# Optimization experiments

Measured on AMD Instinct MI355X. Metric: run time of the kernel, lower is better.

Reference implementation:

```python
import jax, jax.numpy as jnp
import numpy as np

D_MODEL = 2048
N_HEADS = 16
KV_HEADS = 4
HEAD_DIM = D_MODEL // N_HEADS  # 128
GROUPS = N_HEADS // KV_HEADS   # 4
CLIP_QKV = 8.0
EPS = 1e-5
MAX_POS = 2048
ROPE_THETA = 10000.0


def _make_rope(max_pos, dim, theta):
    inv_freq = 1.0 / (theta ** (np.arange(0, dim, 2, dtype=np.float32) / dim))
    t = np.arange(max_pos, dtype=np.float32)
    freqs = np.outer(t, inv_freq)                      # [max_pos, dim/2]
    emb = np.concatenate([freqs, freqs], axis=-1)      # [max_pos, dim]
    return jnp.asarray(np.sin(emb)), jnp.asarray(np.cos(emb))


def setup_inputs() -> dict:
    key = jax.random.key(0)
    ks = jax.random.split(key, 6)
    B, S = 2, 2048
    hidden_states = jax.random.normal(ks[0], (B, S, D_MODEL), dtype=jnp.float32)
    attention_mask = jnp.ones((B, S), dtype=jnp.int32)
    position_ids = jnp.broadcast_to(jnp.arange(S, dtype=jnp.int32)[None, :], (B, S))
    init_std = 0.02
    qkv_out = D_MODEL + 2 * KV_HEADS * HEAD_DIM
    wqkv = jax.random.normal(ks[1], (D_MODEL, qkv_out), dtype=jnp.float32) * init_std
    w_out = jax.random.normal(ks[2], (D_MODEL, D_MODEL), dtype=jnp.float32) * init_std
    norm1_w = jnp.ones((D_MODEL,), dtype=jnp.float32)
    norm2_w = jnp.ones((D_MODEL,), dtype=jnp.float32)
    rope_sin, rope_cos = _make_rope(MAX_POS, HEAD_DIM, ROPE_THETA)
    return {
        'hidden_states': hidden_states,
        'attention_mask': attention_mask,
        'position_ids': position_ids,
        'wqkv': wqkv,
        'w_out': w_out,
        'norm1_w': norm1_w,
        'norm2_w': norm2_w,
        'rope_sin': rope_sin,
        'rope_cos': rope_cos,
    }


def _rmsnorm(x, w, eps=EPS):
    var = jnp.mean(jnp.square(x), axis=-1, keepdims=True)
    return (x * jax.lax.rsqrt(var + eps)) * w


def _rotate_half(x):
    h = x.shape[-1] // 2
    return jnp.concatenate([-x[..., h:], x[..., :h]], axis=-1)


def reference(hidden_states, attention_mask, position_ids, wqkv, w_out, norm1_w, norm2_w, rope_sin, rope_cos):
    B, S, _ = hidden_states.shape
    residual = hidden_states
    # pre-norm
    x = _rmsnorm(hidden_states, norm1_w)
    # fused QKV projection + clip
    qkv = jnp.clip(x @ wqkv, -CLIP_QKV, CLIP_QKV)
    q = qkv[..., :D_MODEL].reshape(B, S, N_HEADS, HEAD_DIM)
    kv_sz = KV_HEADS * HEAD_DIM
    k = qkv[..., D_MODEL:D_MODEL + kv_sz].reshape(B, S, KV_HEADS, HEAD_DIM)
    v = qkv[..., D_MODEL + kv_sz:].reshape(B, S, KV_HEADS, HEAD_DIM)
    # rotary embedding (bshd layout)
    sin = rope_sin[position_ids][:, :, None, :]  # [B,S,1,hd]
    cos = rope_cos[position_ids][:, :, None, :]
    q = q * cos + _rotate_half(q) * sin
    k = k * cos + _rotate_half(k) * sin
    # GQA head repeat
    k = jnp.repeat(k, GROUPS, axis=2)  # [B,S,H,hd]
    v = jnp.repeat(v, GROUPS, axis=2)
    # attention
    scale = 1.0 / jnp.sqrt(jnp.float32(HEAD_DIM))
    scores = jnp.einsum('bqhd,bkhd->bhqk', q, k) * scale
    causal = jnp.tril(jnp.ones((S, S), dtype=bool))
    mask = causal[None, None, :, :] & (attention_mask[:, None, None, :] > 0)
    scores = jnp.where(mask, scores, jnp.finfo(scores.dtype).min)
    probs = jax.nn.softmax(scores, axis=-1)
    attn = jnp.einsum('bhqk,bkhd->bqhd', probs, v).reshape(B, S, D_MODEL)
    attn = attn @ w_out
    # residual add (resid dropout deterministic -> identity) + post-norm
    hidden = residual + attn
    residual_out = hidden
    post = _rmsnorm(hidden, norm2_w)
    return residual_out, post
```

## Files before the change

kernel.cpp:

```cpp
#include <hip/hip_runtime.h>
#include <cstdint>
#include <cstddef>

#define D_MODEL 2048
#define SEQ     2048
#define NB      2
#define ROWS    4096
#define QKV_N   3072
#define NH      16
#define NKV     4
#define HD      128
#define EPSV    1e-5f
#define QPRE    (0.08838834764831845f * 1.4426950408889634f)

typedef unsigned short ushort_t;
typedef __attribute__((ext_vector_type(8))) short  short8;
typedef __attribute__((ext_vector_type(4))) short  short4v;
typedef __attribute__((ext_vector_type(4))) float  floatx4;

__device__ __forceinline__ ushort_t f2b(float f) {
    unsigned u = __float_as_uint(f);
    u += 0x7fffu + ((u >> 16) & 1u);
    return (ushort_t)(u >> 16);
}
__device__ __forceinline__ float b2f(ushort_t u) {
    return __uint_as_float(((unsigned)u) << 16);
}

__device__ __forceinline__ unsigned pkbf(float lo, float hi) {
    unsigned u0 = __float_as_uint(lo) + 0x8000u;
    unsigned u1 = __float_as_uint(hi) + 0x8000u;
    return __builtin_amdgcn_perm(u1, u0, 0x07060302u);
}

#if __has_builtin(__builtin_amdgcn_mfma_f32_16x16x16bf16_1k)
#define HAVE_1K 1
#endif

__device__ __forceinline__ floatx4 pv_mfma(short4v a, short4v b, floatx4 c) {
#ifdef HAVE_1K
    return __builtin_amdgcn_mfma_f32_16x16x16bf16_1k(a, b, c, 0, 0, 0);
#else
    short8 a8 = {a[0], a[1], a[2], a[3], 0, 0, 0, 0};
    short8 b8 = {b[0], b[1], b[2], b[3], 0, 0, 0, 0};
    return __builtin_amdgcn_mfma_f32_16x16x32_bf16(a8, b8, c, 0, 0, 0);
#endif
}

#define GLD_LDS16(gp, lp) __builtin_amdgcn_global_load_lds( \
    (const __attribute__((address_space(1))) void*)(gp),   \
    (__attribute__((address_space(3))) void*)(lp), 16, 0, 0)

__global__ __launch_bounds__(256) void k_rmsnorm_bf16(
        const float* __restrict__ x, const float* __restrict__ w,
        ushort_t* __restrict__ out) {
    int row = blockIdx.x, t = threadIdx.x;
    const float4* xr = (const float4*)(x + (size_t)row * D_MODEL);
    float4 a = xr[t], b = xr[t + 256];
    float ss = a.x*a.x + a.y*a.y + a.z*a.z + a.w*a.w
             + b.x*b.x + b.y*b.y + b.z*b.z + b.w*b.w;
    for (int m = 1; m < 64; m <<= 1) ss += __shfl_xor(ss, m);
    __shared__ float sred[4];
    if ((t & 63) == 0) sred[t >> 6] = ss;
    __syncthreads();
    float r = rsqrtf((sred[0] + sred[1] + sred[2] + sred[3]) * (1.0f / D_MODEL) + EPSV);
    const float4* wr = (const float4*)w;
    float4 wa = wr[t], wb = wr[t + 256];
    ushort4 pa, pb;
    pa.x = f2b(a.x * r * wa.x); pa.y = f2b(a.y * r * wa.y);
    pa.z = f2b(a.z * r * wa.z); pa.w = f2b(a.w * r * wa.w);
    pb.x = f2b(b.x * r * wb.x); pb.y = f2b(b.y * r * wb.y);
    pb.z = f2b(b.z * r * wb.z); pb.w = f2b(b.w * r * wb.w);
    ushort4* o = (ushort4*)(out + (size_t)row * D_MODEL);
    o[t] = pa; o[t + 256] = pb;
}

__global__ __launch_bounds__(256) void k_rmsnorm_f32(
        const float* __restrict__ x, const float* __restrict__ w,
        float* __restrict__ out) {
    int row = blockIdx.x, t = threadIdx.x;
    const float4* xr = (const float4*)(x + (size_t)row * D_MODEL);
    float4 a = xr[t], b = xr[t + 256];
    float ss = a.x*a.x + a.y*a.y + a.z*a.z + a.w*a.w
             + b.x*b.x + b.y*b.y + b.z*b.z + b.w*b.w;
    for (int m = 1; m < 64; m <<= 1) ss += __shfl_xor(ss, m);
    __shared__ float sred[4];
    if ((t & 63) == 0) sred[t >> 6] = ss;
    __syncthreads();
    float r = rsqrtf((sred[0] + sred[1] + sred[2] + sred[3]) * (1.0f / D_MODEL) + EPSV);
    const float4* wr = (const float4*)w;
    float4 wa = wr[t], wb = wr[t + 256];
    float4 oa, ob;
    oa.x = a.x * r * wa.x; oa.y = a.y * r * wa.y; oa.z = a.z * r * wa.z; oa.w = a.w * r * wa.w;
    ob.x = b.x * r * wb.x; ob.y = b.y * r * wb.y; ob.z = b.z * r * wb.z; ob.w = b.w * r * wb.w;
    float4* o = (float4*)(out + (size_t)row * D_MODEL);
    o[t] = oa; o[t + 256] = ob;
}

__global__ __launch_bounds__(256) void k_transpose_cvt(
        const float* __restrict__ in, ushort_t* __restrict__ out, int R, int C) {
    __shared__ float tile[32][33];
    int bc = blockIdx.x * 32, br = blockIdx.y * 32;
    int t = threadIdx.x, lr = t >> 5, lc = t & 31;
    for (int i = 0; i < 4; i++)
        tile[lr + i * 8][lc] = in[(size_t)(br + lr + i * 8) * C + bc + lc];
    __syncthreads();
    for (int i = 0; i < 4; i++)
        out[(size_t)(bc + lr + i * 8) * R + br + lc] = f2b(tile[lc][lr + i * 8]);
}

template <int MODE>
__global__ __launch_bounds__(256) void k_gemm(
        const ushort_t* __restrict__ A, const ushort_t* __restrict__ Bt,
        void* __restrict__ Cout, const float* __restrict__ resid,
        int M, int N, int K) {
    __shared__ __align__(16) ushort_t sA[128 * 32];
    __shared__ __align__(16) ushort_t sB[128 * 32];
    int bm = blockIdx.y * 128, bn = blockIdx.x * 128;
    int t = threadIdx.x;
    int wv = t >> 6, lane = t & 63;
    int wm = (wv >> 1) * 64, wn = (wv & 1) * 64;
    int q4 = lane >> 4, n16 = lane & 15;

    int srow = lane >> 2, scol = (lane & 3) * 8;
    const ushort_t* gA0 = A  + (size_t)(bm + wv * 32 + srow) * K + scol;
    const ushort_t* gA1 = gA0 + (size_t)16 * K;
    const ushort_t* gB0 = Bt + (size_t)(bn + wv * 32 + srow) * K + scol;
    const ushort_t* gB1 = gB0 + (size_t)16 * K;
    ushort_t* lA0 = sA + wv * 1024;
    ushort_t* lA1 = lA0 + 512;
    ushort_t* lB0 = sB + wv * 1024;
    ushort_t* lB1 = lB0 + 512;

    floatx4 zero4 = {0.0f, 0.0f, 0.0f, 0.0f};
    floatx4 acc[4][4];
    for (int i = 0; i < 4; i++)
        for (int j = 0; j < 4; j++) acc[i][j] = zero4;

    for (int k0 = 0; k0 < K; k0 += 32) {
        GLD_LDS16(gA0 + k0, lA0);
        GLD_LDS16(gA1 + k0, lA1);
        GLD_LDS16(gB0 + k0, lB0);
        GLD_LDS16(gB1 + k0, lB1);
        __syncthreads();
        short8 af[4], bfr[4];
        for (int i = 0; i < 4; i++) af[i]  = *(const short8*)&sA[(wm + i * 16 + n16) * 32 + q4 * 8];
        for (int j = 0; j < 4; j++) bfr[j] = *(const short8*)&sB[(wn + j * 16 + n16) * 32 + q4 * 8];
        for (int i = 0; i < 4; i++)
            for (int j = 0; j < 4; j++)
                acc[i][j] = __builtin_amdgcn_mfma_f32_16x16x32_bf16(af[i], bfr[j], acc[i][j], 0, 0, 0);
        __syncthreads();
    }

    for (int i = 0; i < 4; i++) {
        int rbase = bm + wm + i * 16 + q4 * 4;
        for (int j = 0; j < 4; j++) {
            int col = bn + wn + j * 16 + n16;
            if (MODE == 0) {
                ushort_t* C = (ushort_t*)Cout;
                for (int r = 0; r < 4; r++) {
                    float v = acc[i][j][r];
                    v = fminf(fmaxf(v, -8.0f), 8.0f);
                    C[(size_t)(rbase + r) * N + col] = f2b(v);
                }
            } else {
                float* C = (float*)Cout;
                for (int r = 0; r < 4; r++) {
                    float v = acc[i][j][r] + resid[(size_t)(rbase + r) * N + col];
                    C[(size_t)(rbase + r) * N + col] = v;
                }
            }
        }
    }
}

__global__ __launch_bounds__(256) void k_rope(
        const ushort_t* __restrict__ qkv, const int* __restrict__ pos_ids,
        const float* __restrict__ rsin, const float* __restrict__ rcos,
        ushort_t* __restrict__ qout, ushort_t* __restrict__ kout) {
    int wid  = blockIdx.x * 4 + (threadIdx.x >> 6);
    int lane = threadIdx.x & 63;
    int row = wid / 20, slot = wid - row * 20;
    int b = row >> 11, s = row & 2047;
    int pos = pos_ids[row];
    int col0 = (slot < 16) ? slot * HD : D_MODEL + (slot - 16) * HD;
    const ushort_t* src = qkv + (size_t)row * QKV_N + col0;
    float xl = b2f(src[lane]);
    float xh = b2f(src[lane + 64]);
    const float* cp = rcos + (size_t)pos * HD;
    const float* sp = rsin + (size_t)pos * HD;
    float cl = cp[lane], sl = sp[lane];
    float ch = cp[lane + 64], sh = sp[lane + 64];
    float mul = (slot < 16) ? QPRE : 1.0f;
    float ol = (xl * cl - xh * sl) * mul;
    float oh = (xh * ch + xl * sh) * mul;
    if (slot < 16) {
        size_t dst = ((size_t)(b * NH + slot) * SEQ + s) * HD;
        qout[dst + lane] = f2b(ol); qout[dst + lane + 64] = f2b(oh);
    } else {
        size_t dst = ((size_t)(b * NKV + (slot - 16)) * SEQ + s) * HD;
        kout[dst + lane] = f2b(ol); kout[dst + lane + 64] = f2b(oh);
    }
}

__global__ __launch_bounds__(256) void k_vtrans(
        const ushort_t* __restrict__ qkv, ushort_t* __restrict__ vt) {
    __shared__ ushort_t tile[32][33];
    int bh = blockIdx.z;
    int b = bh >> 2, h = bh & 3;
    int s0 = blockIdx.x * 32, d0 = blockIdx.y * 32;
    int t = threadIdx.x, lr = t >> 5, lc = t & 31;
    int col0 = D_MODEL + NKV * HD + h * HD;
    for (int i = 0; i < 4; i++)
        tile[lr + i * 8][lc] =
            qkv[((size_t)b * SEQ + s0 + lr + i * 8) * QKV_N + col0 + d0 + lc];
    __syncthreads();
    for (int i = 0; i < 4; i++)
        vt[((size_t)bh * HD + d0 + lr + i * 8) * SEQ + s0 + lc] = tile[lc][lr + i * 8];
}

__global__ __launch_bounds__(256, 2) void k_attn(
        const ushort_t* __restrict__ Q, const ushort_t* __restrict__ Kr,
        const ushort_t* __restrict__ Vt, const int* __restrict__ amask,
        ushort_t* __restrict__ O) {
    int bidx = blockIdx.x;
    int qt = (SEQ / 64 - 1) - (bidx >> 5);
    int bh = bidx & 31, h = bh & 15, b = bh >> 4;
    int wave = threadIdx.x >> 6, lane = threadIdx.x & 63;
    int q4 = lane >> 4, n16 = lane & 15;

    __shared__ __align__(16) ushort_t sK[2][64 * 128];
    __shared__ __align__(16) ushort_t sV[2][128 * 64];

    const ushort_t* Qh = Q  + (size_t)bh * SEQ * HD;
    const ushort_t* Kh = Kr + (size_t)(b * NKV + (h >> 2)) * SEQ * HD;
    const ushort_t* Vh = Vt + (size_t)(b * NKV + (h >> 2)) * HD * SEQ;
    const int* am = amask + b * SEQ;

    int q0 = qt * 64 + wave * 16;
    int qcol = q0 + n16;

    short8 qf[4];
    for (int kk = 0; kk < 4; kk++)
        qf[kk] = *(const short8*)(Qh + (size_t)qcol * HD + kk * 32 + q4 * 8);

    floatx4 zero4 = {0.0f, 0.0f, 0.0f, 0.0f};
    floatx4 o_acc[8];
    for (int dt = 0; dt < 8; dt++) o_acc[dt] = zero4;
    float m_i = -INFINITY, l_i = 0.0f;

    int krow_l = (lane >> 4);
    int kc_l   = lane & 15;
    int vrow_l = (lane >> 3);
    int vc_l   = lane & 7;

    auto stage_kv = [&](int buf, int kv0) {
        #pragma unroll
        for (int t = 0; t < 4; t++) {
            int krow = wave * 16 + t * 4 + krow_l;
            int kc   = kc_l ^ (krow & 7);
            GLD_LDS16(Kh + (size_t)(kv0 + krow) * HD + kc * 8,
                      &sK[buf][(wave * 16 + t * 4) * 128]);
            int vrow = wave * 32 + t * 8 + vrow_l;
            int vc   = vc_l ^ (vrow & 7);
            GLD_LDS16(Vh + (size_t)vrow * SEQ + kv0 + vc * 8,
                      &sV[buf][(wave * 32 + t * 8) * 64]);
        }
    };

    int kv_iters = qt + 1;

    stage_kv(0, 0);
    asm volatile("s_waitcnt vmcnt(0)" ::: "memory");
    __builtin_amdgcn_s_barrier();
    __builtin_amdgcn_sched_barrier(0);

    for (int it = 0; it < kv_iters; it++) {
        int cur = it & 1;
        int kv0 = it * 64;
        if (it + 1 < kv_iters)
            stage_kv(cur ^ 1, kv0 + 64);

        const ushort_t* sKc = sK[cur];
        const ushort_t* sVc = sV[cur];

        bool tail = (kv0 + 63 > q0);
        floatx4 st[4];
        for (int jj = 0; jj < 4; jj++) st[jj] = zero4;
        for (int jj = 0; jj < 4; jj++) {
            int krow = jj * 16 + n16;
            int sw = krow & 7;
            const ushort_t* kb = sKc + krow * 128;
            for (int kk = 0; kk < 4; kk++) {
                short8 kf = *(const short8*)(kb + ((kk * 4 + q4) ^ sw) * 8);
                st[jj] = __builtin_amdgcn_mfma_f32_16x16x32_bf16(kf, qf[kk], st[jj], 0, 0, 0);
            }
        }
        for (int jj = 0; jj < 4; jj++) {
            int kvb = kv0 + jj * 16 + q4 * 4;
            int4 am4 = *(const int4*)(am + kvb);
            int amr[4] = {am4.x, am4.y, am4.z, am4.w};
            if (tail) {
                for (int r = 0; r < 4; r++)
                    st[jj][r] = (amr[r] > 0 && kvb + r <= qcol) ? st[jj][r] : -1e30f;
            } else {
                for (int r = 0; r < 4; r++)
                    st[jj][r] = (amr[r] > 0) ? st[jj][r] : -1e30f;
            }
        }
        float mx = st[0][0];
        for (int jj = 0; jj < 4; jj++)
            for (int r = 0; r < 4; r++) mx = fmaxf(mx, st[jj][r]);
        mx = fmaxf(mx, __shfl_xor(mx, 16));
        mx = fmaxf(mx, __shfl_xor(mx, 32));
        if (!__all(mx - m_i <= 8.0f)) {
            float mnew = fmaxf(m_i, mx);
            float al = exp2f(m_i - mnew);
            m_i = mnew;
            l_i *= al;
            for (int dt = 0; dt < 8; dt++)
                o_acc[dt] *= al;
        }
        float rs = 0.0f;
        for (int jj = 0; jj < 4; jj++)
            for (int r = 0; r < 4; r++) {
                float p = exp2f(st[jj][r] - m_i);
                st[jj][r] = p;
                rs += p;
            }
        rs += __shfl_xor(rs, 16);
        rs += __shfl_xor(rs, 32);
        l_i += rs;
        for (int jj = 0; jj < 4; jj++) {
            union { unsigned u[2]; short4v s; } uu;
            uu.u[0] = pkbf(st[jj][0], st[jj][1]);
            uu.u[1] = pkbf(st[jj][2], st[jj][3]);
            short4v pfr = uu.s;
            int ch = jj * 2 + (q4 >> 1), hh = q4 & 1;
            for (int dt = 0; dt < 8; dt++) {
                int vrow = dt * 16 + n16;
                short4v vf = *(const short4v*)(sVc + vrow * 64 + ((ch ^ (vrow & 7)) * 8) + hh * 4);
                o_acc[dt] = pv_mfma(vf, pfr, o_acc[dt]);
            }
        }
        asm volatile("s_waitcnt vmcnt(0)" ::: "memory");
        __builtin_amdgcn_s_barrier();
        __builtin_amdgcn_sched_barrier(0);
    }
    float inv = 1.0f / l_i;
    ushort_t* orow = O + ((size_t)(b * SEQ) + qcol) * D_MODEL + h * HD + q4 * 4;
    for (int dt = 0; dt < 8; dt++) {
        uint2 pk;
        pk.x = pkbf(o_acc[dt][0] * inv, o_acc[dt][1] * inv);
        pk.y = pkbf(o_acc[dt][2] * inv, o_acc[dt][3] * inv);
        *(uint2*)(orow + dt * 16) = pk;
    }
}

extern "C" void kernel_launch(void* const* d_in, const int* in_sizes, int n_in,
                              void* d_out, int out_size, void* d_ws, size_t ws_size,
                              hipStream_t stream) {
    const float* hidden = (const float*)d_in[0];
    const int*   amask  = (const int*)d_in[1];
    const int*   pos    = (const int*)d_in[2];
    const float* wqkv   = (const float*)d_in[3];
    const float* wout   = (const float*)d_in[4];
    const float* n1w    = (const float*)d_in[5];
    const float* n2w    = (const float*)d_in[6];
    const float* rsin   = (const float*)d_in[7];
    const float* rcos   = (const float*)d_in[8];
    float* out0 = (float*)d_out;
    float* out1 = out0 + (size_t)ROWS * D_MODEL;

    char* ws = (char*)d_ws;
    ushort_t* x_bf    = (ushort_t*)ws;  ws += (size_t)ROWS * D_MODEL * 2;
    ushort_t* wqkv_t  = (ushort_t*)ws;  ws += (size_t)QKV_N * D_MODEL * 2;
    ushort_t* wout_t  = (ushort_t*)ws;  ws += (size_t)D_MODEL * D_MODEL * 2;
    ushort_t* qkv     = (ushort_t*)ws;  ws += (size_t)ROWS * QKV_N * 2;
    ushort_t* qrot    = (ushort_t*)ws;  ws += (size_t)NB * NH * SEQ * HD * 2;
    ushort_t* krot    = (ushort_t*)ws;  ws += (size_t)NB * NKV * SEQ * HD * 2;
    ushort_t* vt      = (ushort_t*)ws;  ws += (size_t)NB * NKV * HD * SEQ * 2;
    ushort_t* attn    = (ushort_t*)ws;  ws += (size_t)ROWS * D_MODEL * 2;

    k_rmsnorm_bf16<<<ROWS, 256, 0, stream>>>(hidden, n1w, x_bf);
    k_transpose_cvt<<<dim3(QKV_N / 32, D_MODEL / 32), 256, 0, stream>>>(wqkv, wqkv_t, D_MODEL, QKV_N);
    k_transpose_cvt<<<dim3(D_MODEL / 32, D_MODEL / 32), 256, 0, stream>>>(wout, wout_t, D_MODEL, D_MODEL);
    k_gemm<0><<<dim3(QKV_N / 128, ROWS / 128), 256, 0, stream>>>(x_bf, wqkv_t, qkv, nullptr, ROWS, QKV_N, D_MODEL);
    k_rope<<<ROWS * 20 / 4, 256, 0, stream>>>(qkv, pos, rsin, rcos, qrot, krot);
    k_vtrans<<<dim3(SEQ / 32, HD / 32, NB * NKV), 256, 0, stream>>>(qkv, vt);
    k_attn<<<(SEQ / 64) * 32, 256, 0, stream>>>(qrot, krot, vt, amask, attn);
    k_gemm<1><<<dim3(D_MODEL / 128, ROWS / 128), 256, 0, stream>>>(attn, wout_t, out0, hidden, ROWS, D_MODEL, D_MODEL);
    k_rmsnorm_f32<<<ROWS, 256, 0, stream>>>(out0, n2w, out1);
}
```

Measured before the change: 392.4 us.

## Pair short and long causal query tiles per attention block to balance work

Each attention block now processes two query tiles, p and 31-p, so every block does the same total causal work, and the grid halves to 512 blocks. Each K/V tile staged in LDS is reused for both query tiles while both are active. The aim is to remove the load imbalance and tail effect of the triangular causal workload and to cut K/V staging traffic. In exchange, each thread holds doubled accumulators and Q fragments, which raises register pressure and may lower occupancy under the existing launch bounds of 2.

```diff
diff --git a/kernel.cpp b/kernel.cpp
--- a/kernel.cpp
+++ b/kernel.cpp
@@ -224,7 +224,7 @@
         const ushort_t* __restrict__ Vt, const int* __restrict__ amask,
         ushort_t* __restrict__ O) {
     int bidx = blockIdx.x;
-    int qt = (SEQ / 64 - 1) - (bidx >> 5);
+    int p = bidx >> 5;
     int bh = bidx & 31, h = bh & 15, b = bh >> 4;
     int wave = threadIdx.x >> 6, lane = threadIdx.x & 63;
     int q4 = lane >> 4, n16 = lane & 15;
@@ -237,17 +237,21 @@
     const ushort_t* Vh = Vt + (size_t)(b * NKV + (h >> 2)) * HD * SEQ;
     const int* am = amask + b * SEQ;
 
-    int q0 = qt * 64 + wave * 16;
-    int qcol = q0 + n16;
-
-    short8 qf[4];
-    for (int kk = 0; kk < 4; kk++)
-        qf[kk] = *(const short8*)(Qh + (size_t)qcol * HD + kk * 32 + q4 * 8);
+    int qA0 = p * 64 + wave * 16;
+    int qB0 = (31 - p) * 64 + wave * 16;
+    int qcolA = qA0 + n16, qcolB = qB0 + n16;
+
+    short8 qfA[4], qfB[4];
+    for (int kk = 0; kk < 4; kk++) {
+        qfA[kk] = *(const short8*)(Qh + (size_t)qcolA * HD + kk * 32 + q4 * 8);
+        qfB[kk] = *(const short8*)(Qh + (size_t)qcolB * HD + kk * 32 + q4 * 8);
+    }
 
     floatx4 zero4 = {0.0f, 0.0f, 0.0f, 0.0f};
-    floatx4 o_acc[8];
-    for (int dt = 0; dt < 8; dt++) o_acc[dt] = zero4;
-    float m_i = -INFINITY, l_i = 0.0f;
+    floatx4 oA[8], oB[8];
+    for (int dt = 0; dt < 8; dt++) { oA[dt] = zero4; oB[dt] = zero4; }
+    float mA = -INFINITY, lA = 0.0f;
+    float mB = -INFINITY, lB = 0.0f;
 
     int krow_l = (lane >> 4);
     int kc_l   = lane & 15;
@@ -268,7 +272,7 @@
         }
     };
 
-    int kv_iters = qt + 1;
+    int kv_iters = 32 - p;
 
     stage_kv(0, 0);
     asm volatile("s_waitcnt vmcnt(0)" ::: "memory");
@@ -284,76 +288,157 @@
         const ushort_t* sKc = sK[cur];
         const ushort_t* sVc = sV[cur];
 
-        bool tail = (kv0 + 63 > q0);
-        floatx4 st[4];
-        for (int jj = 0; jj < 4; jj++) st[jj] = zero4;
-        for (int jj = 0; jj < 4; jj++) {
-            int krow = jj * 16 + n16;
-            int sw = krow & 7;
-            const ushort_t* kb = sKc + krow * 128;
-            for (int kk = 0; kk < 4; kk++) {
-                short8 kf = *(const short8*)(kb + ((kk * 4 + q4) ^ sw) * 8);
-                st[jj] = __builtin_amdgcn_mfma_f32_16x16x32_bf16(kf, qf[kk], st[jj], 0, 0, 0);
+        bool activeA = (kv0 <= qA0 + 15);
+        bool tailA = (kv0 + 63 > qA0);
+        bool tailB = (kv0 + 63 > qB0);
+
+        floatx4 stA[4], stB[4];
+        for (int jj = 0; jj < 4; jj++) { stA[jj] = zero4; stB[jj] = zero4; }
+
+        if (activeA) {
+            for (int jj = 0; jj < 4; jj++) {
+                int krow = jj * 16 + n16;
+                int sw = krow & 7;
+                const ushort_t* kb = sKc + krow * 128;
+                for (int kk = 0; kk < 4; kk++) {
+                    short8 kf = *(const short8*)(kb + ((kk * 4 + q4) ^ sw) * 8);
+                    stB[jj] = __builtin_amdgcn_mfma_f32_16x16x32_bf16(kf, qfB[kk], stB[jj], 0, 0, 0);
+                    stA[jj] = __builtin_amdgcn_mfma_f32_16x16x32_bf16(kf, qfA[kk], stA[jj], 0, 0, 0);
+                }
+            }
+        } else {
+            for (int jj = 0; jj < 4; jj++) {
+                int krow = jj * 16 + n16;
+                int sw = krow & 7;
+                const ushort_t* kb = sKc + krow * 128;
+                for (int kk = 0; kk < 4; kk++) {
+                    short8 kf = *(const short8*)(kb + ((kk * 4 + q4) ^ sw) * 8);
+                    stB[jj] = __builtin_amdgcn_mfma_f32_16x16x32_bf16(kf, qfB[kk], stB[jj], 0, 0, 0);
+                }
             }
         }
         for (int jj = 0; jj < 4; jj++) {
             int kvb = kv0 + jj * 16 + q4 * 4;
             int4 am4 = *(const int4*)(am + kvb);
             int amr[4] = {am4.x, am4.y, am4.z, am4.w};
-            if (tail) {
+            if (tailB) {
                 for (int r = 0; r < 4; r++)
-                    st[jj][r] = (amr[r] > 0 && kvb + r <= qcol) ? st[jj][r] : -1e30f;
+                    stB[jj][r] = (amr[r] > 0 && kvb + r <= qcolB) ? stB[jj][r] : -1e30f;
             } else {
                 for (int r = 0; r < 4; r++)
-                    st[jj][r] = (amr[r] > 0) ? st[jj][r] : -1e30f;
-            }
-        }
-        float mx = st[0][0];
-        for (int jj = 0; jj < 4; jj++)
-            for (int r = 0; r < 4; r++) mx = fmaxf(mx, st[jj][r]);
-        mx = fmaxf(mx, __shfl_xor(mx, 16));
-        mx = fmaxf(mx, __shfl_xor(mx, 32));
-        if (!__all(mx - m_i <= 8.0f)) {
-            float mnew = fmaxf(m_i, mx);
-            float al = exp2f(m_i - mnew);
-            m_i = mnew;
-            l_i *= al;
-            for (int dt = 0; dt < 8; dt++)
-                o_acc[dt] *= al;
-        }
-        float rs = 0.0f;
-        for (int jj = 0; jj < 4; jj++)
-            for (int r = 0; r < 4; r++) {
-                float p = exp2f(st[jj][r] - m_i);
-                st[jj][r] = p;
-                rs += p;
-            }
-        rs += __shfl_xor(rs, 16);
-        rs += __shfl_xor(rs, 32);
-        l_i += rs;
-        for (int jj = 0; jj < 4; jj++) {
-            union { unsigned u[2]; short4v s; } uu;
-            uu.u[0] = pkbf(st[jj][0], st[jj][1]);
-            uu.u[1] = pkbf(st[jj][2], st[jj][3]);
-            short4v pfr = uu.s;
-            int ch = jj * 2 + (q4 >> 1), hh = q4 & 1;
-            for (int dt = 0; dt < 8; dt++) {
-                int vrow = dt * 16 + n16;
-                short4v vf = *(const short4v*)(sVc + vrow * 64 + ((ch ^ (vrow & 7)) * 8) + hh * 4);
-                o_acc[dt] = pv_mfma(vf, pfr, o_acc[dt]);
+                    stB[jj][r] = (amr[r] > 0) ? stB[jj][r] : -1e30f;
+            }
+            if (activeA) {
+                if (tailA) {
+                    for (int r = 0; r < 4; r++)
+                        stA[jj][r] = (amr[r] > 0 && kvb + r <= qcolA) ? stA[jj][r] : -1e30f;
+                } else {
+                    for (int r = 0; r < 4; r++)
+                        stA[jj][r] = (amr[r] > 0) ? stA[jj][r] : -1e30f;
+                }
+            }
+        }
+        {
+            float mx = stB[0][0];
+            for (int jj = 0; jj < 4; jj++)
+                for (int r = 0; r < 4; r++) mx = fmaxf(mx, stB[jj][r]);
+            mx = fmaxf(mx, __shfl_xor(mx, 16));
+            mx = fmaxf(mx, __shfl_xor(mx, 32));
+            if (!__all(mx - mB <= 8.0f)) {
+                float mnew = fmaxf(mB, mx);
+                float al = exp2f(mB - mnew);
+                mB = mnew;
+                lB *= al;
+                for (int dt = 0; dt < 8; dt++) oB[dt] *= al;
+            }
+            float rs = 0.0f;
+            for (int jj = 0; jj < 4; jj++)
+                for (int r = 0; r < 4; r++) {
+                    float px = exp2f(stB[jj][r] - mB);
+                    stB[jj][r] = px;
+                    rs += px;
+                }
+            rs += __shfl_xor(rs, 16);
+            rs += __shfl_xor(rs, 32);
+            lB += rs;
+        }
+        if (activeA) {
+            float mx = stA[0][0];
+            for (int jj = 0; jj < 4; jj++)
+                for (int r = 0; r < 4; r++) mx = fmaxf(mx, stA[jj][r]);
+            mx = fmaxf(mx, __shfl_xor(mx, 16));
+            mx = fmaxf(mx, __shfl_xor(mx, 32));
+            if (!__all(mx - mA <= 8.0f)) {
+                float mnew = fmaxf(mA, mx);
+                float al = exp2f(mA - mnew);
+                mA = mnew;
+                lA *= al;
+                for (int dt = 0; dt < 8; dt++) oA[dt] *= al;
+            }
+            float rs = 0.0f;
+            for (int jj = 0; jj < 4; jj++)
+                for (int r = 0; r < 4; r++) {
+                    float px = exp2f(stA[jj][r] - mA);
+                    stA[jj][r] = px;
+                    rs += px;
+                }
+            rs += __shfl_xor(rs, 16);
+            rs += __shfl_xor(rs, 32);
+            lA += rs;
+        }
+        if (activeA) {
+            for (int jj = 0; jj < 4; jj++) {
+                union { unsigned u[2]; short4v s; } ub, ua;
+                ub.u[0] = pkbf(stB[jj][0], stB[jj][1]);
+                ub.u[1] = pkbf(stB[jj][2], stB[jj][3]);
+                ua.u[0] = pkbf(stA[jj][0], stA[jj][1]);
+                ua.u[1] = pkbf(stA[jj][2], stA[jj][3]);
+                short4v pfrB = ub.s, pfrA = ua.s;
+                int ch = jj * 2 + (q4 >> 1), hh = q4 & 1;
+                for (int dt = 0; dt < 8; dt++) {
+                    int vrow = dt * 16 + n16;
+                    short4v vf = *(const short4v*)(sVc + vrow * 64 + ((ch ^ (vrow & 7)) * 8) + hh * 4);
+                    oB[dt] = pv_mfma(vf, pfrB, oB[dt]);
+                    oA[dt] = pv_mfma(vf, pfrA, oA[dt]);
+                }
+            }
+        } else {
+            for (int jj = 0; jj < 4; jj++) {
+                union { unsigned u[2]; short4v s; } ub;
+                ub.u[0] = pkbf(stB[jj][0], stB[jj][1]);
+                ub.u[1] = pkbf(stB[jj][2], stB[jj][3]);
+                short4v pfrB = ub.s;
+                int ch = jj * 2 + (q4 >> 1), hh = q4 & 1;
+                for (int dt = 0; dt < 8; dt++) {
+                    int vrow = dt * 16 + n16;
+                    short4v vf = *(const short4v*)(sVc + vrow * 64 + ((ch ^ (vrow & 7)) * 8) + hh * 4);
+                    oB[dt] = pv_mfma(vf, pfrB, oB[dt]);
+                }
             }
         }
         asm volatile("s_waitcnt vmcnt(0)" ::: "memory");
         __builtin_amdgcn_s_barrier();
         __builtin_amdgcn_sched_barrier(0);
     }
-    float inv = 1.0f / l_i;
-    ushort_t* orow = O + ((size_t)(b * SEQ) + qcol) * D_MODEL + h * HD + q4 * 4;
-    for (int dt = 0; dt < 8; dt++) {
-        uint2 pk;
-        pk.x = pkbf(o_acc[dt][0] * inv, o_acc[dt][1] * inv);
-        pk.y = pkbf(o_acc[dt][2] * inv, o_acc[dt][3] * inv);
-        *(uint2*)(orow + dt * 16) = pk;
+    {
+        float inv = 1.0f / lA;
+        ushort_t* orow = O + ((size_t)(b * SEQ) + qcolA) * D_MODEL + h * HD + q4 * 4;
+        for (int dt = 0; dt < 8; dt++) {
+            uint2 pk;
+            pk.x = pkbf(oA[dt][0] * inv, oA[dt][1] * inv);
+            pk.y = pkbf(oA[dt][2] * inv, oA[dt][3] * inv);
+            *(uint2*)(orow + dt * 16) = pk;
+        }
+    }
+    {
+        float inv = 1.0f / lB;
+        ushort_t* orow = O + ((size_t)(b * SEQ) + qcolB) * D_MODEL + h * HD + q4 * 4;
+        for (int dt = 0; dt < 8; dt++) {
+            uint2 pk;
+            pk.x = pkbf(oB[dt][0] * inv, oB[dt][1] * inv);
+            pk.y = pkbf(oB[dt][2] * inv, oB[dt][3] * inv);
+            *(uint2*)(orow + dt * 16) = pk;
+        }
     }
 }
 
@@ -388,7 +473,7 @@
     k_gemm<0><<<dim3(QKV_N / 128, ROWS / 128), 256, 0, stream>>>(x_bf, wqkv_t, qkv, nullptr, ROWS, QKV_N, D_MODEL);
     k_rope<<<ROWS * 20 / 4, 256, 0, stream>>>(qkv, pos, rsin, rcos, qrot, krot);
     k_vtrans<<<dim3(SEQ / 32, HD / 32, NB * NKV), 256, 0, stream>>>(qkv, vt);
-    k_attn<<<(SEQ / 64) * 32, 256, 0, stream>>>(qrot, krot, vt, amask, attn);
+    k_attn<<<16 * 32, 256, 0, stream>>>(qrot, krot, vt, amask, attn);
     k_gemm<1><<<dim3(D_MODEL / 128, ROWS / 128), 256, 0, stream>>>(attn, wout_t, out0, hidden, ROWS, D_MODEL, D_MODEL);
     k_rmsnorm_f32<<<ROWS, 256, 0, stream>>>(out0, n2w, out1);
 }
```

Result: no change. 398.8 us (+1.6%).

## Fuse RoPE and V transpose into QKV GEMM epilogue via LDS staging

Applied to the files above, without the earlier changes.

The QKV GEMM epilogue now stages the clipped bf16 tile in shared memory, then applies rotary embedding and Q prescaling per head-sized column block. It writes Q/K directly in head-major layout and writes V transposed. This removes the intermediate qkv buffer plus the separate rope and vtrans kernels, saving a global round trip and two launches. The cost is a larger shared-memory footprint in the QKV GEMM, about 34 KB, which may lower occupancy, plus an extra epilogue barrier.

```diff
diff --git a/kernel.cpp b/kernel.cpp
--- a/kernel.cpp
+++ b/kernel.cpp
@@ -113,9 +113,12 @@
 __global__ __launch_bounds__(256) void k_gemm(
         const ushort_t* __restrict__ A, const ushort_t* __restrict__ Bt,
         void* __restrict__ Cout, const float* __restrict__ resid,
-        int M, int N, int K) {
-    __shared__ __align__(16) ushort_t sA[128 * 32];
-    __shared__ __align__(16) ushort_t sB[128 * 32];
+        const int* __restrict__ pos_ids, const float* __restrict__ rsin,
+        const float* __restrict__ rcos, ushort_t* __restrict__ kout,
+        ushort_t* __restrict__ vout, int M, int N, int K) {
+    __shared__ __align__(16) ushort_t smem[MODE == 0 ? (128 * 136) : (128 * 64)];
+    ushort_t* sA = smem;
+    ushort_t* sB = smem + 128 * 32;
     int bm = blockIdx.y * 128, bn = blockIdx.x * 128;
     int t = threadIdx.x;
     int wv = t >> 6, lane = t & 63;
@@ -152,18 +155,11 @@
         __syncthreads();
     }
 
-    for (int i = 0; i < 4; i++) {
-        int rbase = bm + wm + i * 16 + q4 * 4;
-        for (int j = 0; j < 4; j++) {
-            int col = bn + wn + j * 16 + n16;
-            if (MODE == 0) {
-                ushort_t* C = (ushort_t*)Cout;
-                for (int r = 0; r < 4; r++) {
-                    float v = acc[i][j][r];
-                    v = fminf(fmaxf(v, -8.0f), 8.0f);
-                    C[(size_t)(rbase + r) * N + col] = f2b(v);
-                }
-            } else {
+    if (MODE == 1) {
+        for (int i = 0; i < 4; i++) {
+            int rbase = bm + wm + i * 16 + q4 * 4;
+            for (int j = 0; j < 4; j++) {
+                int col = bn + wn + j * 16 + n16;
                 float* C = (float*)Cout;
                 for (int r = 0; r < 4; r++) {
                     float v = acc[i][j][r] + resid[(size_t)(rbase + r) * N + col];
@@ -171,52 +167,91 @@
                 }
             }
         }
-    }
-}
-
-__global__ __launch_bounds__(256) void k_rope(
-        const ushort_t* __restrict__ qkv, const int* __restrict__ pos_ids,
-        const float* __restrict__ rsin, const float* __restrict__ rcos,
-        ushort_t* __restrict__ qout, ushort_t* __restrict__ kout) {
-    int wid  = blockIdx.x * 4 + (threadIdx.x >> 6);
-    int lane = threadIdx.x & 63;
-    int row = wid / 20, slot = wid - row * 20;
-    int b = row >> 11, s = row & 2047;
-    int pos = pos_ids[row];
-    int col0 = (slot < 16) ? slot * HD : D_MODEL + (slot - 16) * HD;
-    const ushort_t* src = qkv + (size_t)row * QKV_N + col0;
-    float xl = b2f(src[lane]);
-    float xh = b2f(src[lane + 64]);
-    const float* cp = rcos + (size_t)pos * HD;
-    const float* sp = rsin + (size_t)pos * HD;
-    float cl = cp[lane], sl = sp[lane];
-    float ch = cp[lane + 64], sh = sp[lane + 64];
-    float mul = (slot < 16) ? QPRE : 1.0f;
-    float ol = (xl * cl - xh * sl) * mul;
-    float oh = (xh * ch + xl * sh) * mul;
-    if (slot < 16) {
-        size_t dst = ((size_t)(b * NH + slot) * SEQ + s) * HD;
-        qout[dst + lane] = f2b(ol); qout[dst + lane + 64] = f2b(oh);
+        return;
+    }
+
+    const int TP = 136;
+    for (int i = 0; i < 4; i++) {
+        int lrow = wm + i * 16 + q4 * 4;
+        for (int j = 0; j < 4; j++) {
+            int lcol = wn + j * 16 + n16;
+            for (int r = 0; r < 4; r++) {
+                float v = fminf(fmaxf(acc[i][j][r], -8.0f), 8.0f);
+                smem[(lrow + r) * TP + lcol] = f2b(v);
+            }
+        }
+    }
+    __syncthreads();
+
+    int head = bn >> 7;
+    if (head < 20) {
+        int lr = t >> 1;
+        int row_g = bm + lr;
+        int b = row_g >> 11, s = row_g & 2047;
+        int pos = pos_ids[row_g];
+        int dbase = (t & 1) * 32;
+        const float* cp = rcos + (size_t)pos * HD;
+        const float* sp = rsin + (size_t)pos * HD;
+        float mul = (head < 16) ? QPRE : 1.0f;
+        ushort_t* dst;
+        if (head < 16)
+            dst = (ushort_t*)Cout + ((size_t)(b * NH + head) * SEQ + s) * HD;
+        else
+            dst = kout + ((size_t)(b * NKV + (head - 16)) * SEQ + s) * HD;
+        for (int c = 0; c < 4; c++) {
+            int d = dbase + c * 8;
+            short8 xl8 = *(const short8*)&smem[lr * TP + d];
+            short8 xh8 = *(const short8*)&smem[lr * TP + d + 64];
+            float4 cl0 = *(const float4*)(cp + d);
+            float4 cl1 = *(const float4*)(cp + d + 4);
+            float4 sl0 = *(const float4*)(sp + d);
+            float4 sl1 = *(const float4*)(sp + d + 4);
+            float4 ch0 = *(const float4*)(cp + d + 64);
+            float4 ch1 = *(const float4*)(cp + d + 68);
+            float4 sh0 = *(const float4*)(sp + d + 64);
+            float4 sh1 = *(const float4*)(sp + d + 68);
+            float cl[8] = {cl0.x, cl0.y, cl0.z, cl0.w, cl1.x, cl1.y, cl1.z, cl1.w};
+            float sl[8] = {sl0.x, sl0.y, sl0.z, sl0.w, sl1.x, sl1.y, sl1.z, sl1.w};
+            float ch[8] = {ch0.x, ch0.y, ch0.z, ch0.w, ch1.x, ch1.y, ch1.z, ch1.w};
+            float sh[8] = {sh0.x, sh0.y, sh0.z, sh0.w, sh1.x, sh1.y, sh1.z, sh1.w};
+            ushort_t ol[8], oh[8];
+            for (int k2 = 0; k2 < 8; k2++) {
+                float xl = b2f((ushort_t)xl8[k2]);
+                float xh = b2f((ushort_t)xh8[k2]);
+                ol[k2] = f2b((xl * cl[k2] - xh * sl[k2]) * mul);
+                oh[k2] = f2b((xh * ch[k2] + xl * sh[k2]) * mul);
+            }
+            uint4 pl, ph;
+            pl.x = (unsigned)ol[0] | ((unsigned)ol[1] << 16);
+            pl.y = (unsigned)ol[2] | ((unsigned)ol[3] << 16);
+            pl.z = (unsigned)ol[4] | ((unsigned)ol[5] << 16);
+            pl.w = (unsigned)ol[6] | ((unsigned)ol[7] << 16);
+            ph.x = (unsigned)oh[0] | ((unsigned)oh[1] << 16);
+            ph.y = (unsigned)oh[2] | ((unsigned)oh[3] << 16);
+            ph.z = (unsigned)oh[4] | ((unsigned)oh[5] << 16);
+            ph.w = (unsigned)oh[6] | ((unsigned)oh[7] << 16);
+            *(uint4*)(dst + d) = pl;
+            *(uint4*)(dst + d + 64) = ph;
+        }
     } else {
-        size_t dst = ((size_t)(b * NKV + (slot - 16)) * SEQ + s) * HD;
-        kout[dst + lane] = f2b(ol); kout[dst + lane + 64] = f2b(oh);
-    }
-}
-
-__global__ __launch_bounds__(256) void k_vtrans(
-        const ushort_t* __restrict__ qkv, ushort_t* __restrict__ vt) {
-    __shared__ ushort_t tile[32][33];
-    int bh = blockIdx.z;
-    int b = bh >> 2, h = bh & 3;
-    int s0 = blockIdx.x * 32, d0 = blockIdx.y * 32;
-    int t = threadIdx.x, lr = t >> 5, lc = t & 31;
-    int col0 = D_MODEL + NKV * HD + h * HD;
-    for (int i = 0; i < 4; i++)
-        tile[lr + i * 8][lc] =
-            qkv[((size_t)b * SEQ + s0 + lr + i * 8) * QKV_N + col0 + d0 + lc];
-    __syncthreads();
-    for (int i = 0; i < 4; i++)
-        vt[((size_t)bh * HD + d0 + lr + i * 8) * SEQ + s0 + lc] = tile[lc][lr + i * 8];
+        int vslot = head - 20;
+        int d = t >> 1;
+        int s0l = (t & 1) * 64;
+        int b = bm >> 11;
+        int sbase = (bm & 2047) + s0l;
+        ushort_t* dst = vout + ((size_t)(b * NKV + vslot) * HD + d) * SEQ + sbase;
+        for (int c = 0; c < 8; c++) {
+            unsigned v8[8];
+            for (int k2 = 0; k2 < 8; k2++)
+                v8[k2] = smem[(s0l + c * 8 + k2) * TP + d];
+            uint4 w;
+            w.x = v8[0] | (v8[1] << 16);
+            w.y = v8[2] | (v8[3] << 16);
+            w.z = v8[4] | (v8[5] << 16);
+            w.w = v8[6] | (v8[7] << 16);
+            *(uint4*)(dst + c * 8) = w;
+        }
+    }
 }
 
 __global__ __launch_bounds__(256, 2) void k_attn(
@@ -376,7 +411,6 @@
     ushort_t* x_bf    = (ushort_t*)ws;  ws += (size_t)ROWS * D_MODEL * 2;
     ushort_t* wqkv_t  = (ushort_t*)ws;  ws += (size_t)QKV_N * D_MODEL * 2;
     ushort_t* wout_t  = (ushort_t*)ws;  ws += (size_t)D_MODEL * D_MODEL * 2;
-    ushort_t* qkv     = (ushort_t*)ws;  ws += (size_t)ROWS * QKV_N * 2;
     ushort_t* qrot    = (ushort_t*)ws;  ws += (size_t)NB * NH * SEQ * HD * 2;
     ushort_t* krot    = (ushort_t*)ws;  ws += (size_t)NB * NKV * SEQ * HD * 2;
     ushort_t* vt      = (ushort_t*)ws;  ws += (size_t)NB * NKV * HD * SEQ * 2;
@@ -385,10 +419,10 @@
     k_rmsnorm_bf16<<<ROWS, 256, 0, stream>>>(hidden, n1w, x_bf);
     k_transpose_cvt<<<dim3(QKV_N / 32, D_MODEL / 32), 256, 0, stream>>>(wqkv, wqkv_t, D_MODEL, QKV_N);
     k_transpose_cvt<<<dim3(D_MODEL / 32, D_MODEL / 32), 256, 0, stream>>>(wout, wout_t, D_MODEL, D_MODEL);
-    k_gemm<0><<<dim3(QKV_N / 128, ROWS / 128), 256, 0, stream>>>(x_bf, wqkv_t, qkv, nullptr, ROWS, QKV_N, D_MODEL);
-    k_rope<<<ROWS * 20 / 4, 256, 0, stream>>>(qkv, pos, rsin, rcos, qrot, krot);
-    k_vtrans<<<dim3(SEQ / 32, HD / 32, NB * NKV), 256, 0, stream>>>(qkv, vt);
+    k_gemm<0><<<dim3(QKV_N / 128, ROWS / 128), 256, 0, stream>>>(
+        x_bf, wqkv_t, qrot, nullptr, pos, rsin, rcos, krot, vt, ROWS, QKV_N, D_MODEL);
     k_attn<<<(SEQ / 64) * 32, 256, 0, stream>>>(qrot, krot, vt, amask, attn);
-    k_gemm<1><<<dim3(D_MODEL / 128, ROWS / 128), 256, 0, stream>>>(attn, wout_t, out0, hidden, ROWS, D_MODEL, D_MODEL);
+    k_gemm<1><<<dim3(D_MODEL / 128, ROWS / 128), 256, 0, stream>>>(
+        attn, wout_t, out0, hidden, nullptr, nullptr, nullptr, nullptr, nullptr, ROWS, D_MODEL, D_MODEL);
     k_rmsnorm_f32<<<ROWS, 256, 0, stream>>>(out0, n2w, out1);
 }
```

Result: slower. 417.4 us (+6.4%).

## Double GEMM K-tile to 64 and XOR-swizzle LDS layout

Applied to the files above, without the earlier changes.

The bf16 GEMM kernel now stages a 64-wide K slice per iteration instead of 32, which halves the number of barrier pairs over the K loop. The shared-memory tile uses an XOR swizzle of 16-byte chunks by row so fragment reads avoid LDS bank conflicts. The global-to-LDS load addresses are permuted to match the swizzle. LDS use doubles to 32 KB per block, which may lower occupancy.

```diff
diff --git a/kernel.cpp b/kernel.cpp
--- a/kernel.cpp
+++ b/kernel.cpp
@@ -114,41 +114,48 @@
         const ushort_t* __restrict__ A, const ushort_t* __restrict__ Bt,
         void* __restrict__ Cout, const float* __restrict__ resid,
         int M, int N, int K) {
-    __shared__ __align__(16) ushort_t sA[128 * 32];
-    __shared__ __align__(16) ushort_t sB[128 * 32];
+    __shared__ __align__(16) ushort_t sA[128 * 64];
+    __shared__ __align__(16) ushort_t sB[128 * 64];
     int bm = blockIdx.y * 128, bn = blockIdx.x * 128;
     int t = threadIdx.x;
     int wv = t >> 6, lane = t & 63;
     int wm = (wv >> 1) * 64, wn = (wv & 1) * 64;
     int q4 = lane >> 4, n16 = lane & 15;
 
-    int srow = lane >> 2, scol = (lane & 3) * 8;
-    const ushort_t* gA0 = A  + (size_t)(bm + wv * 32 + srow) * K + scol;
-    const ushort_t* gA1 = gA0 + (size_t)16 * K;
-    const ushort_t* gB0 = Bt + (size_t)(bn + wv * 32 + srow) * K + scol;
-    const ushort_t* gB1 = gB0 + (size_t)16 * K;
-    ushort_t* lA0 = sA + wv * 1024;
-    ushort_t* lA1 = lA0 + 512;
-    ushort_t* lB0 = sB + wv * 1024;
-    ushort_t* lB1 = lB0 + 512;
+    int srow8 = lane >> 3;
+    int sxor  = ((lane & 7) ^ srow8) * 8;
+    const ushort_t* gA = A  + (size_t)(bm + wv * 32 + srow8) * K + sxor;
+    const ushort_t* gB = Bt + (size_t)(bn + wv * 32 + srow8) * K + sxor;
+    ushort_t* lA = sA + wv * 32 * 64;
+    ushort_t* lB = sB + wv * 32 * 64;
 
     floatx4 zero4 = {0.0f, 0.0f, 0.0f, 0.0f};
     floatx4 acc[4][4];
     for (int i = 0; i < 4; i++)
         for (int j = 0; j < 4; j++) acc[i][j] = zero4;
 
-    for (int k0 = 0; k0 < K; k0 += 32) {
-        GLD_LDS16(gA0 + k0, lA0);
-        GLD_LDS16(gA1 + k0, lA1);
-        GLD_LDS16(gB0 + k0, lB0);
-        GLD_LDS16(gB1 + k0, lB1);
+    for (int k0 = 0; k0 < K; k0 += 64) {
+        #pragma unroll
+        for (int i = 0; i < 4; i++) {
+            GLD_LDS16(gA + (size_t)(i * 8) * K + k0, lA + i * 8 * 64);
+            GLD_LDS16(gB + (size_t)(i * 8) * K + k0, lB + i * 8 * 64);
+        }
         __syncthreads();
-        short8 af[4], bfr[4];
-        for (int i = 0; i < 4; i++) af[i]  = *(const short8*)&sA[(wm + i * 16 + n16) * 32 + q4 * 8];
-        for (int j = 0; j < 4; j++) bfr[j] = *(const short8*)&sB[(wn + j * 16 + n16) * 32 + q4 * 8];
-        for (int i = 0; i < 4; i++)
-            for (int j = 0; j < 4; j++)
-                acc[i][j] = __builtin_amdgcn_mfma_f32_16x16x32_bf16(af[i], bfr[j], acc[i][j], 0, 0, 0);
+        #pragma unroll
+        for (int kk = 0; kk < 2; kk++) {
+            short8 af[4], bfr[4];
+            for (int i = 0; i < 4; i++) {
+                int row = wm + i * 16 + n16;
+                af[i]  = *(const short8*)&sA[row * 64 + (((kk * 4 + q4) ^ (row & 7)) * 8)];
+            }
+            for (int j = 0; j < 4; j++) {
+                int row = wn + j * 16 + n16;
+                bfr[j] = *(const short8*)&sB[row * 64 + (((kk * 4 + q4) ^ (row & 7)) * 8)];
+            }
+            for (int i = 0; i < 4; i++)
+                for (int j = 0; j < 4; j++)
+                    acc[i][j] = __builtin_amdgcn_mfma_f32_16x16x32_bf16(af[i], bfr[j], acc[i][j], 0, 0, 0);
+        }
         __syncthreads();
     }
 
```

After: 379.7 us. -3.2%, faster.
